# Optimization experiments

Measured on AMD Instinct MI355X. Metric: run time of the kernel, lower is better.

## Reference

```python
import jax, jax.numpy as jnp
import numpy as np

NUM_BITS = 10
MEM_SIZE = 2 ** NUM_BITS  # 1024
HIDDEN = 1024
INPUT = 1024
BATCH = 16384
LN_EPS = 1e-5


def setup_inputs() -> dict:
    key = jax.random.key(0)
    ks = jax.random.split(key, 8)
    s = 0.02
    return {
        "x": jax.random.normal(ks[0], (BATCH, INPUT), jnp.float32),
        "h_prev": jax.random.normal(ks[1], (BATCH, HIDDEN), jnp.float32),
        "memory": jax.random.normal(ks[2], (MEM_SIZE, HIDDEN), jnp.float32),
        "W_w": jax.random.normal(ks[3], (HIDDEN, INPUT), jnp.float32) * s,
        "W_b": jnp.zeros((HIDDEN,), jnp.float32),
        "U_w": jax.random.normal(ks[4], (HIDDEN, HIDDEN), jnp.float32) * s,
        "U_b": jnp.zeros((HIDDEN,), jnp.float32),
        "Q_w": jax.random.normal(ks[5], (HIDDEN, HIDDEN), jnp.float32) * s,
        "Q_b": jnp.zeros((HIDDEN,), jnp.float32),
        "M_w": jax.random.normal(ks[6], (NUM_BITS, HIDDEN), jnp.float32) * s,
        "M_b": jnp.zeros((NUM_BITS,), jnp.float32),
        "ln_g": jnp.ones((HIDDEN,), jnp.float32),
        "ln_b": jnp.zeros((HIDDEN,), jnp.float32),
    }


def reference(x, h_prev, memory, W_w, W_b, U_w, U_b, Q_w, Q_b, M_w, M_b, ln_g, ln_b):
    # Binary address from h_prev (eval-mode hard threshold, non-differentiable)
    powers = jnp.asarray(2 ** np.arange(NUM_BITS - 1, -1, -1), dtype=x.dtype)  # [num_bits]
    logits = h_prev @ M_w.T + M_b                              # [B, num_bits]
    binary = (jax.nn.sigmoid(logits) > 0.5).astype(x.dtype)    # hard bits
    index = jnp.clip((binary * powers).sum(-1).astype(jnp.int32), 0, MEM_SIZE - 1)  # [B]
    h_mem = memory[index]                                      # gather [B, H]
    # Fused linear combine + LayerNorm + sigmoid
    pre = x @ W_w.T + W_b + h_prev @ U_w.T + U_b + h_mem @ Q_w.T + Q_b  # [B, H]
    mu = pre.mean(-1, keepdims=True)
    var = ((pre - mu) ** 2).mean(-1, keepdims=True)            # biased var (torch LN)
    norm = (pre - mu) * jax.lax.rsqrt(var + LN_EPS)
    return jax.nn.sigmoid(norm * ln_g + ln_b)                  # h_new [B, H]
```

## Files before the change

### kernel.cpp

```cpp
#include <hip/hip_runtime.h>

#define BATCH   16384
#define HIDDEN  1024
#define K2      2048
#define MEMSZ   1024
#define NBITS   10

#define BM 256
#define BN 256
#define BK 64
#define NT (K2 / BK)

#define BBLK    2048
#define U_BM    262144
#define U_TOT   2359296
#define SBLK    2304
#define SSTRIDE (SBLK * 256)

typedef __bf16 bf16x8 __attribute__((ext_vector_type(8)));
typedef float  f32x4  __attribute__((ext_vector_type(4)));
typedef unsigned short u16x8 __attribute__((ext_vector_type(8)));

__device__ __forceinline__ unsigned short f2bf(float f) {
    unsigned int u = __float_as_uint(f);
    u += 0x7FFFu + ((u >> 16) & 1u);
    return (unsigned short)(u >> 16);
}

__device__ __forceinline__ u16x8 f2bf8(float4 a, float4 b) {
    u16x8 r;
    r[0] = f2bf(a.x); r[1] = f2bf(a.y); r[2] = f2bf(a.z); r[3] = f2bf(a.w);
    r[4] = f2bf(b.x); r[5] = f2bf(b.y); r[6] = f2bf(b.z); r[7] = f2bf(b.w);
    return r;
}

__device__ __forceinline__ ushort4 f2bf4(float4 a) {
    ushort4 r;
    r.x = f2bf(a.x); r.y = f2bf(a.y); r.z = f2bf(a.z); r.w = f2bf(a.w);
    return r;
}

__device__ __forceinline__ void gload_lds16(const void* g, void* l) {
    __builtin_amdgcn_global_load_lds(
        (const __attribute__((address_space(1))) unsigned int*)g,
        (__attribute__((address_space(3))) unsigned int*)l,
        16, 0, 0);
}

__global__ __launch_bounds__(256) void front_kernel(
        const float* __restrict__ W, const float* __restrict__ U,
        const float* __restrict__ x, const float* __restrict__ h_prev,
        const float* __restrict__ M_w, const float* __restrict__ M_b,
        unsigned short* __restrict__ Bm, unsigned short* __restrict__ A,
        int* __restrict__ idxbuf) {
    if (blockIdx.x < BBLK) {
        const int wv   = threadIdx.x >> 6;
        const int lane = threadIdx.x & 63;
        const int row0 = (blockIdx.x * 4 + wv) * 2;
        const int c4   = lane * 4;

        float4 h[2][4];
#pragma unroll
        for (int r = 0; r < 2; ++r) {
            const float* hr = h_prev + (size_t)(row0 + r) * HIDDEN;
#pragma unroll
            for (int seg = 0; seg < 4; ++seg)
                h[r][seg] = *reinterpret_cast<const float4*>(hr + seg * 256 + c4);
        }

        float s[2][NBITS];
#pragma unroll
        for (int j = 0; j < NBITS; ++j) {
            const float* mj = M_w + (size_t)j * HIDDEN;
            float4 m[4];
#pragma unroll
            for (int seg = 0; seg < 4; ++seg)
                m[seg] = *reinterpret_cast<const float4*>(mj + seg * 256 + c4);
#pragma unroll
            for (int r = 0; r < 2; ++r) {
                float acc = 0.f;
#pragma unroll
                for (int seg = 0; seg < 4; ++seg)
                    acc += h[r][seg].x * m[seg].x + h[r][seg].y * m[seg].y
                         + h[r][seg].z * m[seg].z + h[r][seg].w * m[seg].w;
                s[r][j] = acc;
            }
        }
#pragma unroll
        for (int off = 32; off >= 1; off >>= 1) {
#pragma unroll
            for (int r = 0; r < 2; ++r)
#pragma unroll
                for (int j = 0; j < NBITS; ++j)
                    s[r][j] += __shfl_xor(s[r][j], off, 64);
        }
#pragma unroll
        for (int r = 0; r < 2; ++r) {
            int idx = 0;
#pragma unroll
            for (int j = 0; j < NBITS; ++j)
                if (s[r][j] + M_b[j] > 0.f) idx |= 1 << (NBITS - 1 - j);
            if (lane == 0) idxbuf[row0 + r] = idx;
        }

#pragma unroll
        for (int r = 0; r < 2; ++r) {
            unsigned short* arow = A + (size_t)(row0 + r) * K2 + 1024;
#pragma unroll
            for (int seg = 0; seg < 4; ++seg)
                *reinterpret_cast<ushort4*>(arow + seg * 256 + c4) = f2bf4(h[r][seg]);
        }
        return;
    }

    const int u0 = (blockIdx.x - BBLK) * 256 + threadIdx.x;
    const float* s4[4];
    unsigned short* d4[4];
#pragma unroll
    for (int i = 0; i < 4; ++i) {
        int u = u0 + i * SSTRIDE;
        if (u < U_BM) {
            int n  = u >> 8;
            int k8 = (u & 255) << 3;
            s4[i] = (k8 < 1024) ? (W + (size_t)n * 1024 + k8)
                                : (U + (size_t)n * 1024 + (k8 - 1024));
            d4[i] = Bm + (size_t)n * K2 + k8;
        } else {
            int e = (u - U_BM) << 3;
            int row = e >> 10, col = e & 1023;
            s4[i] = x + (size_t)row * HIDDEN + col;
            d4[i] = A + (size_t)row * K2 + col;
        }
    }
    float4 va[4], vb[4];
#pragma unroll
    for (int i = 0; i < 4; ++i) {
        va[i] = *reinterpret_cast<const float4*>(s4[i]);
        vb[i] = *reinterpret_cast<const float4*>(s4[i] + 4);
    }
    __builtin_amdgcn_sched_barrier(0);
#pragma unroll
    for (int i = 0; i < 4; ++i)
        *reinterpret_cast<u16x8*>(d4[i]) = f2bf8(va[i], vb[i]);
}

__global__ __launch_bounds__(256) void mq_kernel(
        const float* __restrict__ memory,
        const float* __restrict__ Q,
        float* __restrict__ MQ) {
    __shared__ unsigned short As[128 * 32];
    __shared__ unsigned short Bs[128 * 32];

    const int ks = blockIdx.x >> 6;
    const int mb = (blockIdx.x >> 3) & 7;
    const int nb = blockIdx.x & 7;
    const int t    = threadIdx.x;
    const int lane = t & 63;
    const int w    = t >> 6;
    const int wr   = w >> 1, wc = w & 1;
    const int rr   = lane & 15, rq = lane >> 4;
    const int srow = t >> 1;
    const int scol = (t & 1) * 16;
    const int swr  = (srow & 3) << 4;

    f32x4 acc[4][4] = {};

    for (int kt = 0; kt < 8; ++kt) {
        const int k0 = ks * 256 + kt * 32;
        const float* ap = memory + (size_t)(mb * 128 + srow) * 1024 + k0 + scol;
        const float* bp = Q      + (size_t)(nb * 128 + srow) * 1024 + k0 + scol;
        float4 a0 = *reinterpret_cast<const float4*>(ap);
        float4 a1 = *reinterpret_cast<const float4*>(ap + 4);
        float4 a2 = *reinterpret_cast<const float4*>(ap + 8);
        float4 a3 = *reinterpret_cast<const float4*>(ap + 12);
        float4 b0 = *reinterpret_cast<const float4*>(bp);
        float4 b1 = *reinterpret_cast<const float4*>(bp + 4);
        float4 b2 = *reinterpret_cast<const float4*>(bp + 8);
        float4 b3 = *reinterpret_cast<const float4*>(bp + 12);
        __syncthreads();
        {
            char* ar = reinterpret_cast<char*>(As) + srow * 64;
            char* br = reinterpret_cast<char*>(Bs) + srow * 64;
            *reinterpret_cast<u16x8*>(ar + ((scol * 2)      ^ swr)) = f2bf8(a0, a1);
            *reinterpret_cast<u16x8*>(ar + ((scol * 2 + 16) ^ swr)) = f2bf8(a2, a3);
            *reinterpret_cast<u16x8*>(br + ((scol * 2)      ^ swr)) = f2bf8(b0, b1);
            *reinterpret_cast<u16x8*>(br + ((scol * 2 + 16) ^ swr)) = f2bf8(b2, b3);
        }
        __syncthreads();
        bf16x8 af[4], bfv[4];
#pragma unroll
        for (int m = 0; m < 4; ++m) {
            int r = wr * 64 + m * 16 + rr;
            af[m] = *reinterpret_cast<const bf16x8*>(
                reinterpret_cast<const char*>(As) + r * 64 + ((rq * 16) ^ ((r & 3) << 4)));
        }
#pragma unroll
        for (int n = 0; n < 4; ++n) {
            int r = wc * 64 + n * 16 + rr;
            bfv[n] = *reinterpret_cast<const bf16x8*>(
                reinterpret_cast<const char*>(Bs) + r * 64 + ((rq * 16) ^ ((r & 3) << 4)));
        }
#pragma unroll
        for (int m = 0; m < 4; ++m)
#pragma unroll
            for (int n = 0; n < 4; ++n)
                acc[m][n] = __builtin_amdgcn_mfma_f32_16x16x32_bf16(
                    af[m], bfv[n], acc[m][n], 0, 0, 0);
    }

#pragma unroll
    for (int m = 0; m < 4; ++m)
#pragma unroll
        for (int n = 0; n < 4; ++n) {
            int gcol = nb * 128 + wc * 64 + n * 16 + rr;
#pragma unroll
            for (int j = 0; j < 4; ++j) {
                int grow = mb * 128 + wr * 64 + m * 16 + rq * 4 + j;
                atomicAdd(&MQ[(size_t)grow * 1024 + gcol], acc[m][n][j]);
            }
        }
}


__device__ __forceinline__ void stage_g(const unsigned short* __restrict__ src,
                                        int rowbase, int kt, int g,
                                        unsigned short* ldsTile, int t) {
    const int o      = g * 8192 + t * 16;
    const int row    = o >> 7;
    const int inner  = o & 127;
    const int sinner = inner ^ ((row & 7) << 4);
    const char* gp = reinterpret_cast<const char*>(
                         src + (size_t)(rowbase + row) * K2 + kt * BK) + sinner;
    gload_lds16(gp, reinterpret_cast<char*>(ldsTile) + o);
}

__device__ __forceinline__ bf16x8 ldsfrag(const unsigned short* tile, int row,
                                          int kbyte_x_sw) {
    return *reinterpret_cast<const bf16x8*>(
        reinterpret_cast<const char*>(tile) + row * 128 + kbyte_x_sw);
}

#define PH_BAR()                                                     \
    do {                                                             \
        asm volatile("" ::: "memory");                               \
        __builtin_amdgcn_s_barrier();                                \
        asm volatile("" ::: "memory");                               \
    } while (0)

#define LGKM(N)                                                      \
    do {                                                             \
        asm volatile("s_waitcnt lgkmcnt(" #N ")" ::: "memory");      \
        __builtin_amdgcn_sched_barrier(0);                           \
    } while (0)

#define MFMA_Q(AF, BF, MB, NB)                                                 \
    {                                                                          \
        __builtin_amdgcn_s_setprio(1);                                         \
        _Pragma("unroll") for (int m_ = 0; m_ < 4; ++m_)                       \
        _Pragma("unroll") for (int n_ = 0; n_ < 2; ++n_)                       \
        _Pragma("unroll") for (int kk_ = 0; kk_ < 2; ++kk_)                    \
            acc[(MB) + m_][(NB) + n_] =                                        \
                __builtin_amdgcn_mfma_f32_16x16x32_bf16(                       \
                    AF[m_][kk_], BF[n_][kk_],                                  \
                    acc[(MB) + m_][(NB) + n_], 0, 0, 0);                       \
        __builtin_amdgcn_s_setprio(0);                                         \
    }

__global__ __launch_bounds__(512, 2) void gemm_kernel(
        const unsigned short* __restrict__ A,
        const unsigned short* __restrict__ Bm,
        float* __restrict__ C) {
    __shared__ alignas(16) unsigned short lds[2][2][BM * BK];

    const int bid  = blockIdx.x;
    const int wgid = (bid & 7) * 32 + (bid >> 3);
    const int mblk = wgid >> 2;
    const int nblk = wgid & 3;

    const int t    = threadIdx.x;
    const int lane = t & 63;
    const int w    = t >> 6;
    const int wr   = w >> 2;
    const int wc   = w & 3;
    const int rr   = lane & 15;
    const int rq   = lane >> 4;
    const int sw   = (rr & 7) << 4;
    const int rqb  = rq * 16;
    const int wrb  = wr * 128;
    const int wcb  = wc * 64;

    const int arow = mblk * BM;
    const int brow = nblk * BN;

    f32x4 acc[8][4] = {};

    {
#pragma unroll
        for (int g = 0; g < 4; ++g) stage_g(A,  arow, 0, g, &lds[0][0][0], t);
#pragma unroll
        for (int g = 0; g < 4; ++g) stage_g(Bm, brow, 0, g, &lds[0][1][0], t);
#pragma unroll
        for (int g = 0; g < 4; ++g) stage_g(Bm, brow, 1, g, &lds[1][1][0], t);
#pragma unroll
        for (int g = 0; g < 4; ++g) stage_g(A,  arow, 1, g, &lds[1][0][0], t);
        asm volatile("s_waitcnt vmcnt(8)" ::: "memory");
        asm volatile("" ::: "memory");
        __builtin_amdgcn_s_barrier();
    }

    bf16x8 af  [4][2];
    bf16x8 af2 [4][2];
    bf16x8 bfr01[2][2];
    bf16x8 bfr23[2][2];

#pragma unroll
    for (int m = 0; m < 4; ++m) {
        af[m][0] = ldsfrag(&lds[0][0][0], wrb + m * 16 + rr, (rqb) ^ sw);
        af[m][1] = ldsfrag(&lds[0][0][0], wrb + m * 16 + rr, (64 + rqb) ^ sw);
    }
#pragma unroll
    for (int n = 0; n < 2; ++n) {
        bfr01[n][0] = ldsfrag(&lds[0][1][0], wcb + n * 16 + rr, (rqb) ^ sw);
        bfr01[n][1] = ldsfrag(&lds[0][1][0], wcb + n * 16 + rr, (64 + rqb) ^ sw);
    }

    for (int kt = 0; kt < NT; ++kt) {
        const int c = kt & 1;
        const unsigned short* At  = &lds[c][0][0];
        const unsigned short* Bt  = &lds[c][1][0];
        const unsigned short* nxA = &lds[c ^ 1][0][0];
        const unsigned short* nxB = &lds[c ^ 1][1][0];
        unsigned short* curA = &lds[c][0][0];
        unsigned short* curB = &lds[c][1][0];
        const bool pf1 = (kt + 1 < NT);
        const bool pf2 = (kt + 2 < NT);

        PH_BAR();
#pragma unroll
        for (int n = 0; n < 2; ++n) {
            bfr23[n][0] = ldsfrag(Bt, wcb + 32 + n * 16 + rr, (rqb) ^ sw);
            bfr23[n][1] = ldsfrag(Bt, wcb + 32 + n * 16 + rr, (64 + rqb) ^ sw);
        }
        af2[0][0] = ldsfrag(At, wrb + 64 + rr, (rqb) ^ sw);
        af2[0][1] = ldsfrag(At, wrb + 64 + rr, (64 + rqb) ^ sw);
        LGKM(6);
        MFMA_Q(af, bfr01, 0, 0);

        PH_BAR();
#pragma unroll
        for (int m = 1; m < 4; ++m) {
            af2[m][0] = ldsfrag(At, wrb + 64 + m * 16 + rr, (rqb) ^ sw);
            af2[m][1] = ldsfrag(At, wrb + 64 + m * 16 + rr, (64 + rqb) ^ sw);
        }
        LGKM(8);
        MFMA_Q(af, bfr23, 0, 2);
        __builtin_amdgcn_sched_barrier(0);
        asm volatile("s_waitcnt vmcnt(0)" ::: "memory");
        asm volatile("" ::: "memory");

        PH_BAR();
        if (pf2) {
            stage_g(Bm, brow, kt + 2, 0, curB, t);
            stage_g(Bm, brow, kt + 2, 1, curB, t);
            stage_g(Bm, brow, kt + 2, 2, curB, t);
            stage_g(Bm, brow, kt + 2, 3, curB, t);
        }
        if (pf1) {
#pragma unroll
            for (int m = 0; m < 3; ++m) {
                af[m][0] = ldsfrag(nxA, wrb + m * 16 + rr, (rqb) ^ sw);
                af[m][1] = ldsfrag(nxA, wrb + m * 16 + rr, (64 + rqb) ^ sw);
            }
            LGKM(6);
        } else {
            LGKM(0);
        }
        MFMA_Q(af2, bfr01, 4, 0);

        PH_BAR();
        if (pf2) {
            stage_g(A, arow, kt + 2, 0, curA, t);
            stage_g(A, arow, kt + 2, 1, curA, t);
            stage_g(A, arow, kt + 2, 2, curA, t);
            stage_g(A, arow, kt + 2, 3, curA, t);
        }
        if (pf1) {
            af[3][0] = ldsfrag(nxA, wrb + 48 + rr, (rqb) ^ sw);
            af[3][1] = ldsfrag(nxA, wrb + 48 + rr, (64 + rqb) ^ sw);
#pragma unroll
            for (int n = 0; n < 2; ++n) {
                bfr01[n][0] = ldsfrag(nxB, wcb + n * 16 + rr, (rqb) ^ sw);
                bfr01[n][1] = ldsfrag(nxB, wcb + n * 16 + rr, (64 + rqb) ^ sw);
            }
        }
        MFMA_Q(af2, bfr23, 4, 2);
    }

#pragma unroll
    for (int mi = 0; mi < 8; ++mi) {
#pragma unroll
        for (int n = 0; n < 4; ++n) {
            const int gcol = nblk * BN + wcb + n * 16 + rr;
#pragma unroll
            for (int j = 0; j < 4; ++j) {
                const int grow = mblk * BM + wrb + mi * 16 + rq * 4 + j;
                C[(size_t)grow * HIDDEN + gcol] = acc[mi][n][j];
            }
        }
    }
}

__global__ __launch_bounds__(256) void ln_kernel(
        float* __restrict__ C,
        const int* __restrict__ idxbuf,
        const float* __restrict__ MQ,
        const float* __restrict__ W_b, const float* __restrict__ U_b,
        const float* __restrict__ Q_b, const float* __restrict__ ln_g,
        const float* __restrict__ ln_b) {
    const int row = blockIdx.x;
    const int t   = threadIdx.x;
    const int midx = idxbuf[row];
    float4* rowp = reinterpret_cast<float4*>(C + (size_t)row * HIDDEN);
    const float4* mqp = reinterpret_cast<const float4*>(MQ + (size_t)midx * HIDDEN);

    float4 p  = rowp[t];
    float4 mq = mqp[t];
    float4 bw = reinterpret_cast<const float4*>(W_b)[t];
    float4 bu = reinterpret_cast<const float4*>(U_b)[t];
    float4 bq = reinterpret_cast<const float4*>(Q_b)[t];
    p.x += mq.x + bw.x + bu.x + bq.x;
    p.y += mq.y + bw.y + bu.y + bq.y;
    p.z += mq.z + bw.z + bu.z + bq.z;
    p.w += mq.w + bw.w + bu.w + bq.w;

    float s  = p.x + p.y + p.z + p.w;
    float sq = p.x * p.x + p.y * p.y + p.z * p.z + p.w * p.w;
#pragma unroll
    for (int off = 32; off >= 1; off >>= 1) {
        s  += __shfl_xor(s,  off, 64);
        sq += __shfl_xor(sq, off, 64);
    }
    __shared__ float red[8];
    const int lane = t & 63, w = t >> 6;
    if (lane == 0) { red[w] = s; red[4 + w] = sq; }
    __syncthreads();
    const float S    = red[0] + red[1] + red[2] + red[3];
    const float SQ   = red[4] + red[5] + red[6] + red[7];
    const float mean = S * (1.0f / HIDDEN);
    const float var  = SQ * (1.0f / HIDDEN) - mean * mean;
    const float rstd = rsqrtf(var + 1e-5f);

    float4 g = reinterpret_cast<const float4*>(ln_g)[t];
    float4 b = reinterpret_cast<const float4*>(ln_b)[t];
    float4 o;
    o.x = 1.f / (1.f + __expf(-((p.x - mean) * rstd * g.x + b.x)));
    o.y = 1.f / (1.f + __expf(-((p.y - mean) * rstd * g.y + b.y)));
    o.z = 1.f / (1.f + __expf(-((p.z - mean) * rstd * g.z + b.z)));
    o.w = 1.f / (1.f + __expf(-((p.w - mean) * rstd * g.w + b.w)));
    rowp[t] = o;
}

extern "C" void kernel_launch(void* const* d_in, const int* in_sizes, int n_in,
                              void* d_out, int out_size, void* d_ws, size_t ws_size,
                              hipStream_t stream) {
    const float* x      = (const float*)d_in[0];
    const float* h_prev = (const float*)d_in[1];
    const float* memory = (const float*)d_in[2];
    const float* W_w    = (const float*)d_in[3];
    const float* W_b    = (const float*)d_in[4];
    const float* U_w    = (const float*)d_in[5];
    const float* U_b    = (const float*)d_in[6];
    const float* Q_w    = (const float*)d_in[7];
    const float* Q_b    = (const float*)d_in[8];
    const float* M_w    = (const float*)d_in[9];
    const float* M_b    = (const float*)d_in[10];
    const float* ln_g   = (const float*)d_in[11];
    const float* ln_b   = (const float*)d_in[12];

    char* ws = (char*)d_ws;
    unsigned short* A   = (unsigned short*)(ws);
    unsigned short* Bm  = (unsigned short*)(ws + 67108864);
    float*          MQ  = (float*)         (ws + 71303168);
    int*            idx = (int*)           (ws + 75497472);

    float* pre = (float*)d_out;

    hipMemsetAsync(MQ, 0, (size_t)MEMSZ * HIDDEN * sizeof(float), stream);
    hipLaunchKernelGGL(mq_kernel, dim3(256), dim3(256), 0, stream,
                       memory, Q_w, MQ);
    hipLaunchKernelGGL(front_kernel, dim3(BBLK + SBLK), dim3(256), 0, stream,
                       W_w, U_w, x, h_prev, M_w, M_b, Bm, A, idx);
    hipLaunchKernelGGL(gemm_kernel, dim3((BATCH / BM) * (HIDDEN / BN)), dim3(512), 0, stream,
                       A, Bm, pre);
    hipLaunchKernelGGL(ln_kernel, dim3(BATCH), dim3(256), 0, stream,
                       pre, idx, MQ, W_b, U_b, Q_b, ln_g, ln_b);
}
```

Measured before the change: 165.3 us.

## Fold memory·Qᵀ precompute into main GEMM launch as extra blocks

```diff
diff --git a/kernel.cpp b/kernel.cpp
--- a/kernel.cpp
+++ b/kernel.cpp
@@ -11,6 +11,7 @@
 #define BK 64
 #define NT (K2 / BK)
 
+#define MQB     256
 #define BBLK    2048
 #define U_BM    262144
 #define U_TOT   2359296
@@ -144,83 +145,6 @@
         *reinterpret_cast<u16x8*>(d4[i]) = f2bf8(va[i], vb[i]);
 }
 
-__global__ __launch_bounds__(256) void mq_kernel(
-        const float* __restrict__ memory,
-        const float* __restrict__ Q,
-        float* __restrict__ MQ) {
-    __shared__ unsigned short As[128 * 32];
-    __shared__ unsigned short Bs[128 * 32];
-
-    const int ks = blockIdx.x >> 6;
-    const int mb = (blockIdx.x >> 3) & 7;
-    const int nb = blockIdx.x & 7;
-    const int t    = threadIdx.x;
-    const int lane = t & 63;
-    const int w    = t >> 6;
-    const int wr   = w >> 1, wc = w & 1;
-    const int rr   = lane & 15, rq = lane >> 4;
-    const int srow = t >> 1;
-    const int scol = (t & 1) * 16;
-    const int swr  = (srow & 3) << 4;
-
-    f32x4 acc[4][4] = {};
-
-    for (int kt = 0; kt < 8; ++kt) {
-        const int k0 = ks * 256 + kt * 32;
-        const float* ap = memory + (size_t)(mb * 128 + srow) * 1024 + k0 + scol;
-        const float* bp = Q      + (size_t)(nb * 128 + srow) * 1024 + k0 + scol;
-        float4 a0 = *reinterpret_cast<const float4*>(ap);
-        float4 a1 = *reinterpret_cast<const float4*>(ap + 4);
-        float4 a2 = *reinterpret_cast<const float4*>(ap + 8);
-        float4 a3 = *reinterpret_cast<const float4*>(ap + 12);
-        float4 b0 = *reinterpret_cast<const float4*>(bp);
-        float4 b1 = *reinterpret_cast<const float4*>(bp + 4);
-        float4 b2 = *reinterpret_cast<const float4*>(bp + 8);
-        float4 b3 = *reinterpret_cast<const float4*>(bp + 12);
-        __syncthreads();
-        {
-            char* ar = reinterpret_cast<char*>(As) + srow * 64;
-            char* br = reinterpret_cast<char*>(Bs) + srow * 64;
-            *reinterpret_cast<u16x8*>(ar + ((scol * 2)      ^ swr)) = f2bf8(a0, a1);
-            *reinterpret_cast<u16x8*>(ar + ((scol * 2 + 16) ^ swr)) = f2bf8(a2, a3);
-            *reinterpret_cast<u16x8*>(br + ((scol * 2)      ^ swr)) = f2bf8(b0, b1);
-            *reinterpret_cast<u16x8*>(br + ((scol * 2 + 16) ^ swr)) = f2bf8(b2, b3);
-        }
-        __syncthreads();
-        bf16x8 af[4], bfv[4];
-#pragma unroll
-        for (int m = 0; m < 4; ++m) {
-            int r = wr * 64 + m * 16 + rr;
-            af[m] = *reinterpret_cast<const bf16x8*>(
-                reinterpret_cast<const char*>(As) + r * 64 + ((rq * 16) ^ ((r & 3) << 4)));
-        }
-#pragma unroll
-        for (int n = 0; n < 4; ++n) {
-            int r = wc * 64 + n * 16 + rr;
-            bfv[n] = *reinterpret_cast<const bf16x8*>(
-                reinterpret_cast<const char*>(Bs) + r * 64 + ((rq * 16) ^ ((r & 3) << 4)));
-        }
-#pragma unroll
-        for (int m = 0; m < 4; ++m)
-#pragma unroll
-            for (int n = 0; n < 4; ++n)
-                acc[m][n] = __builtin_amdgcn_mfma_f32_16x16x32_bf16(
-                    af[m], bfv[n], acc[m][n], 0, 0, 0);
-    }
-
-#pragma unroll
-    for (int m = 0; m < 4; ++m)
-#pragma unroll
-        for (int n = 0; n < 4; ++n) {
-            int gcol = nb * 128 + wc * 64 + n * 16 + rr;
-#pragma unroll
-            for (int j = 0; j < 4; ++j) {
-                int grow = mb * 128 + wr * 64 + m * 16 + rq * 4 + j;
-                atomicAdd(&MQ[(size_t)grow * 1024 + gcol], acc[m][n][j]);
-            }
-        }
-}
-
 
 __device__ __forceinline__ void stage_g(const unsigned short* __restrict__ src,
                                         int rowbase, int kt, int g,
@@ -266,18 +190,91 @@
         __builtin_amdgcn_s_setprio(0);                                         \
     }
 
-__global__ __launch_bounds__(512, 2) void gemm_kernel(
+__global__ __launch_bounds__(512, 2) void gemm_mq_kernel(
         const unsigned short* __restrict__ A,
         const unsigned short* __restrict__ Bm,
+        const float* __restrict__ memory,
+        const float* __restrict__ Q,
+        float* __restrict__ MQ,
         float* __restrict__ C) {
     __shared__ alignas(16) unsigned short lds[2][2][BM * BK];
 
-    const int bid  = blockIdx.x;
-    const int wgid = (bid & 7) * 32 + (bid >> 3);
+    const int bid = blockIdx.x;
+    const int t   = threadIdx.x;
+
+    if (bid < MQB) {
+        unsigned short* As = &lds[0][0][0];
+        unsigned short* Bs = As + 128 * 32;
+
+        const int ks = bid >> 6;
+        const int mb = (bid >> 3) & 7;
+        const int nb = bid & 7;
+        const int lane = t & 63;
+        const int w    = t >> 6;
+        const int wr   = w >> 2, wc = w & 3;
+        const int rr   = lane & 15, rq = lane >> 4;
+        const int srow = t >> 2;
+        const int sc8  = (t & 3) * 8;
+        const int swr  = (srow & 3) << 4;
+
+        f32x4 acc[4][2] = {};
+
+        for (int kt = 0; kt < 8; ++kt) {
+            const int k0 = ks * 256 + kt * 32;
+            const float* ap = memory + (size_t)(mb * 128 + srow) * 1024 + k0 + sc8;
+            const float* bp = Q      + (size_t)(nb * 128 + srow) * 1024 + k0 + sc8;
+            float4 a0 = *reinterpret_cast<const float4*>(ap);
+            float4 a1 = *reinterpret_cast<const float4*>(ap + 4);
+            float4 b0 = *reinterpret_cast<const float4*>(bp);
+            float4 b1 = *reinterpret_cast<const float4*>(bp + 4);
+            __syncthreads();
+            {
+                char* ar = reinterpret_cast<char*>(As) + srow * 64;
+                char* br = reinterpret_cast<char*>(Bs) + srow * 64;
+                *reinterpret_cast<u16x8*>(ar + ((sc8 * 2) ^ swr)) = f2bf8(a0, a1);
+                *reinterpret_cast<u16x8*>(br + ((sc8 * 2) ^ swr)) = f2bf8(b0, b1);
+            }
+            __syncthreads();
+            bf16x8 af[4], bfv[2];
+#pragma unroll
+            for (int m = 0; m < 4; ++m) {
+                int r = wr * 64 + m * 16 + rr;
+                af[m] = *reinterpret_cast<const bf16x8*>(
+                    reinterpret_cast<const char*>(As) + r * 64 + ((rq * 16) ^ ((r & 3) << 4)));
+            }
+#pragma unroll
+            for (int n = 0; n < 2; ++n) {
+                int r = wc * 32 + n * 16 + rr;
+                bfv[n] = *reinterpret_cast<const bf16x8*>(
+                    reinterpret_cast<const char*>(Bs) + r * 64 + ((rq * 16) ^ ((r & 3) << 4)));
+            }
+#pragma unroll
+            for (int m = 0; m < 4; ++m)
+#pragma unroll
+                for (int n = 0; n < 2; ++n)
+                    acc[m][n] = __builtin_amdgcn_mfma_f32_16x16x32_bf16(
+                        af[m], bfv[n], acc[m][n], 0, 0, 0);
+        }
+
+#pragma unroll
+        for (int m = 0; m < 4; ++m)
+#pragma unroll
+            for (int n = 0; n < 2; ++n) {
+                int gcol = nb * 128 + wc * 32 + n * 16 + rr;
+#pragma unroll
+                for (int j = 0; j < 4; ++j) {
+                    int grow = mb * 128 + wr * 64 + m * 16 + rq * 4 + j;
+                    atomicAdd(&MQ[(size_t)grow * 1024 + gcol], acc[m][n][j]);
+                }
+            }
+        return;
+    }
+
+    const int gbid = bid - MQB;
+    const int wgid = (gbid & 7) * 32 + (gbid >> 3);
     const int mblk = wgid >> 2;
     const int nblk = wgid & 3;
 
-    const int t    = threadIdx.x;
     const int lane = t & 63;
     const int w    = t >> 6;
     const int wr   = w >> 2;
@@ -486,12 +483,11 @@
     float* pre = (float*)d_out;
 
     hipMemsetAsync(MQ, 0, (size_t)MEMSZ * HIDDEN * sizeof(float), stream);
-    hipLaunchKernelGGL(mq_kernel, dim3(256), dim3(256), 0, stream,
-                       memory, Q_w, MQ);
     hipLaunchKernelGGL(front_kernel, dim3(BBLK + SBLK), dim3(256), 0, stream,
                        W_w, U_w, x, h_prev, M_w, M_b, Bm, A, idx);
-    hipLaunchKernelGGL(gemm_kernel, dim3((BATCH / BM) * (HIDDEN / BN)), dim3(512), 0, stream,
-                       A, Bm, pre);
+    hipLaunchKernelGGL(gemm_mq_kernel,
+                       dim3(MQB + (BATCH / BM) * (HIDDEN / BN)), dim3(512), 0, stream,
+                       A, Bm, memory, Q_w, MQ, pre);
     hipLaunchKernelGGL(ln_kernel, dim3(BATCH), dim3(256), 0, stream,
                        pre, idx, MQ, W_b, U_b, Q_b, ln_g, ln_b);
 }
```

Result: faster. 160.0 us (-3.2%).
